# Optimization experiments

Hardware: AMD Instinct MI355X
Metric: run time of the kernel (lower is better)

## Reference

```python
import jax, jax.numpy as jnp
import numpy as np

B, T, I, F, M, O = 256, 512, 128, 512, 512, 128


def setup_inputs() -> dict:
    key = jax.random.key(0)
    ks = jax.random.split(key, 12)
    def lin(k, out_d, in_d):
        std = 1.0 / np.sqrt(in_d)
        kw, kb = jax.random.split(k)
        W = jax.random.uniform(kw, (out_d, in_d), jnp.float32, -std, std)
        b = jax.random.uniform(kb, (out_d,), jnp.float32, -std, std)
        return W, b
    Wi2f, bi2f = lin(ks[0], F, I)
    Wm2f, bm2f = lin(ks[1], F, M)
    Wf2m, bf2m = lin(ks[2], M, F)
    Wm2m, bm2m = lin(ks[3], M, M)
    Wout, bout = lin(ks[4], O, M)
    x = jax.random.normal(ks[5], (B, T, I), jnp.float32)
    m0 = jnp.zeros((B, M), jnp.float32)
    return {"x": x, "m0": m0,
            "Wi2f": Wi2f, "bi2f": bi2f, "Wm2f": Wm2f, "bm2f": bm2f,
            "Wf2m": Wf2m, "bf2m": bf2m, "Wm2m": Wm2m, "bm2m": bm2m,
            "Wout": Wout, "bout": bout}


def reference(x, m0, Wi2f, bi2f, Wm2f, bm2f, Wf2m, bf2m, Wm2m, bm2m, Wout, bout):
    # Precompute input->functional projection for all timesteps (batched GEMM).
    xp = jnp.einsum('bti,fi->btf', x, Wi2f) + bi2f  # (B, T, F)

    def step(m, xp_t):
        f = jnp.tanh(xp_t + m @ Wm2f.T + bm2f)           # (B, F)
        m_new = (f @ Wf2m.T + bf2m) + (m @ Wm2m.T + bm2m)  # (B, M)
        return m_new, m_new

    m_last, _ms = jax.lax.scan(step, m0, jnp.swapaxes(xp, 0, 1))  # ms: (T, B, M)
    # OUTPUT_TYPE.LAST_OUT: output layer applied to final memory state.
    return m_last @ Wout.T + bout  # (B, O)
```

## Files before the change

kernel.cpp:

```cpp
#include <hip/hip_runtime.h>
#include <hip/hip_bf16.h>

typedef __bf16 bf16x8 __attribute__((ext_vector_type(8)));
typedef __bf16 bf16x4 __attribute__((ext_vector_type(4)));
typedef float  f32x4  __attribute__((ext_vector_type(4)));
typedef unsigned int u32;
typedef unsigned long long u64;

static __device__ __forceinline__ void mfma_z(f32x4& d, bf16x8 a, const f32x4& b) {
    asm("v_mfma_f32_16x16x32_bf16 %0, %1, %2, 0"
        : "=&v"(d) : "v"(a), "a"(b));
}
static __device__ __forceinline__ void mfma_a(f32x4& d, bf16x8 a, const f32x4& b) {
    asm("v_mfma_f32_16x16x32_bf16 %0, %1, %2, %0"
        : "+v"(d) : "v"(a), "a"(b));
}
#define ACC_GUARD(e, o) asm volatile("s_nop 7\n\ts_nop 7" : "+v"(e), "+v"(o))

static __device__ __forceinline__ f32x4 mfma16(bf16x8 a, bf16x8 b, f32x4 c) {
    return __builtin_amdgcn_mfma_f32_16x16x32_bf16(a, b, c, 0, 0, 0);
}

static __device__ __forceinline__ void poll_flags(const u32* flags, u32 tgt,
                                                  int lane, u32& alive) {
    if (!alive) return;
    for (u32 it = 0; it < (1u << 22); ++it) {
        u32 v = __hip_atomic_load(&flags[lane & 7], __ATOMIC_RELAXED, __HIP_MEMORY_SCOPE_AGENT);
        if (__all((int)(v >= tgt))) return;
    }
    alive = 0;
}

#define TLEN 512
#define IDIM 128
#define FDIM 512
#define MDIM 512
#define ODIM 128
#define BC   16
#define NGRP 16
#define NCU  8
#define PSTR 520
#define XSTR 136
#define SSTR 20

#define WS_WI   0
#define WS_W2F  (WS_WI  + FDIM*IDIM*2)
#define WS_W2M  (WS_W2F + FDIM*MDIM*2)
#define WS_WF2  (WS_W2M + MDIM*MDIM*2)
#define WS_WO   (WS_WF2 + MDIM*FDIM*2)
#define WS_C    (WS_WO  + ODIM*MDIM*2)
#define WS_D    (WS_C   + FDIM*FDIM*2)
#define WS_B1   (WS_D   + MDIM*FDIM*2)
#define WS_B23  (WS_B1  + FDIM*4)
#define WS_CB   (WS_B23 + MDIM*4)
#define WS_CU   (WS_CB  + FDIM*4)
#define WS_FLG  (WS_CU  + MDIM*4)
#define WS_BUF  (WS_FLG + NGRP*64*4)

#define N_WI  (FDIM*IDIM)
#define N_W2F (FDIM*MDIM)
#define N_W2M (MDIM*MDIM)
#define N_WF2 (MDIM*FDIM)
#define N_WO  (ODIM*MDIM)

__global__ __launch_bounds__(256) void lmn_prep1(
    const float* __restrict__ Wi2f, const float* __restrict__ Wm2f,
    const float* __restrict__ Wm2m, const float* __restrict__ Wf2m,
    const float* __restrict__ Wout,
    const float* __restrict__ bi2f, const float* __restrict__ bm2f,
    const float* __restrict__ bf2m, const float* __restrict__ bm2m,
    __bf16* __restrict__ WI, __bf16* __restrict__ W2F, __bf16* __restrict__ W2M,
    __bf16* __restrict__ WF2, __bf16* __restrict__ WO,
    float* __restrict__ b1, float* __restrict__ b23, u32* __restrict__ flags)
{
    int i = blockIdx.x * 256 + threadIdx.x;
    if (i < N_WI)  { WI[i]  = (__bf16)Wi2f[i]; return; }  i -= N_WI;
    if (i < N_W2F) { W2F[i] = (__bf16)Wm2f[i]; return; }  i -= N_W2F;
    if (i < N_W2M) { W2M[i] = (__bf16)Wm2m[i]; return; }  i -= N_W2M;
    if (i < N_WF2) { WF2[i] = (__bf16)Wf2m[i]; return; }  i -= N_WF2;
    if (i < N_WO)  { WO[i]  = (__bf16)Wout[i]; return; }  i -= N_WO;
    if (i < FDIM)  { b1[i]  = bi2f[i] + bm2f[i]; return; } i -= FDIM;
    if (i < MDIM)  { b23[i] = bf2m[i] + bm2m[i]; return; } i -= MDIM;
    if (i < NGRP * 64) { flags[i] = 0u; return; }
}

__global__ __launch_bounds__(256) void lmn_prep2(
    const float* __restrict__ Wm2f, const float* __restrict__ Wm2m,
    const float* __restrict__ Wf2m,
    const float* __restrict__ b1, const float* __restrict__ b23,
    __bf16* __restrict__ C, __bf16* __restrict__ D,
    float* __restrict__ cb, float* __restrict__ cu)
{
    int bb = blockIdx.x;
    if (bb < 2048) {
        int row = bb >> 1;
        int k   = (bb & 1) * 256 + threadIdx.x;
        const float* A = (row < 512) ? Wm2f : Wm2m;
        int r = row & 511;
        float acc = 0.f;
        for (int j = 0; j < 512; ++j)
            acc += A[(size_t)r * 512 + j] * Wf2m[(size_t)j * 512 + k];
        if (row < 512) C[(size_t)r * 512 + k] = (__bf16)acc;
        else           D[(size_t)r * 512 + k] = (__bf16)acc;
        return;
    }
    int idx = (bb - 2048) * 256 + threadIdx.x;
    if (idx < 512) {
        float acc = b1[idx];
        for (int j = 0; j < 512; ++j) acc += Wm2f[(size_t)idx * 512 + j] * b23[j];
        cb[idx] = acc;
    } else {
        int r = idx - 512;
        float acc = 0.f;
        for (int j = 0; j < 512; ++j) acc += Wm2m[(size_t)r * 512 + j] * b23[j];
        cu[r] = acc;
    }
}

__global__ __launch_bounds__(512, 2) void lmn_scan(
    const float* __restrict__ x, const float* __restrict__ m0,
    const __bf16* __restrict__ WI, const __bf16* __restrict__ W2F,
    const __bf16* __restrict__ W2M, const __bf16* __restrict__ Cm,
    const __bf16* __restrict__ Dm, const __bf16* __restrict__ WF2,
    const __bf16* __restrict__ WO,
    const float* __restrict__ b1, const float* __restrict__ cb,
    const float* __restrict__ cu, const float* __restrict__ b23,
    const float* __restrict__ bout,
    u32* __restrict__ flags_all, __bf16* __restrict__ buf,
    float* __restrict__ out)
{
    __shared__ __bf16 ulds[BC][PSTR];
    __shared__ __bf16 flds[BC][PSTR];
    __shared__ __bf16 xlds[BC][XSTR];
    __shared__ __bf16 sstg[8][BC][SSTR];

    const int tid  = threadIdx.x;
    const int lane = tid & 63;
    const int w    = tid >> 6;
    const int wq   = w & 3;
    const int l15  = lane & 15;
    const int l4   = lane >> 4;
    const int koff = 8 * l4;
    const bool sRole = (w < 4);

    const int b = blockIdx.x;
    const int g = b & 15;
    const int p = b >> 4;
    const int row0 = g * BC;

    u32* flags = flags_all + g * 64;
    u32  alive = 1;

    const int c0 = 64 * p + 16 * wq + l15;

    f32x4 wgt[36];
    {
        const __bf16* rA = (sRole ? W2F : W2M) + (size_t)c0 * MDIM;
        const __bf16* rC = (sRole ? Cm  : Dm ) + (size_t)c0 * FDIM;
        #pragma unroll
        for (int j = 0; j < 16; ++j) {
            wgt[j]      = *(const f32x4*)&rA[j * 32 + koff];
            wgt[16 + j] = *(const f32x4*)&rC[j * 32 + koff];
        }
        if (sRole) {
            const __bf16* rX = WI + (size_t)c0 * IDIM;
            #pragma unroll
            for (int j = 0; j < 4; ++j) wgt[32 + j] = *(const f32x4*)&rX[j * 32 + koff];
        } else {
            #pragma unroll
            for (int j = 32; j < 36; ++j) wgt[j] = f32x4{0, 0, 0, 0};
        }
        #pragma unroll
        for (int j = 0; j < 36; ++j) asm volatile("" : "+a"(wgt[j]));
    }
    const float b1r = sRole ? b1[c0] : 0.f;
    const float cbr = sRole ? cb[c0] : 0.f;
    const float cur = sRole ? 0.f    : cu[c0];

    #pragma unroll
    for (int i = 0; i < 2; ++i) {
        int c = tid + 512 * i;
        int row = c >> 6, col8 = (c & 63) << 3;
        const float* ms = &m0[(size_t)(row0 + row) * MDIM + col8];
        float4 v0 = ((const float4*)ms)[0], v1 = ((const float4*)ms)[1];
        *(bf16x8*)&ulds[row][col8] =
            bf16x8{(__bf16)v0.x, (__bf16)v0.y, (__bf16)v0.z, (__bf16)v0.w,
                   (__bf16)v1.x, (__bf16)v1.y, (__bf16)v1.z, (__bf16)v1.w};
    }
    if (tid < 256) {
        int rr = tid >> 4, c8 = (tid & 15) << 3;
        const float* xs = &x[(size_t)(row0 + rr) * TLEN * IDIM + c8];
        float4 v0 = ((const float4*)xs)[0], v1 = ((const float4*)xs)[1];
        *(bf16x8*)&xlds[rr][c8] =
            bf16x8{(__bf16)v0.x, (__bf16)v0.y, (__bf16)v0.z, (__bf16)v0.w,
                   (__bf16)v1.x, (__bf16)v1.y, (__bf16)v1.z, (__bf16)v1.w};
    }
    __syncthreads();

    f32x4 accE, accO;
    {
        bf16x8 a0 = *(const bf16x8*)&ulds[l15][0 * 32 + koff];
        bf16x8 a1 = *(const bf16x8*)&ulds[l15][1 * 32 + koff];
        mfma_z(accE, a0, wgt[0]);  mfma_z(accO, a1, wgt[1]);
        #pragma unroll
        for (int j = 2; j < 16; ++j) {
            bf16x8 am = *(const bf16x8*)&ulds[l15][j * 32 + koff];
            if (j & 1) mfma_a(accO, am, wgt[j]);
            else       mfma_a(accE, am, wgt[j]);
        }
        if (sRole) {
            #pragma unroll
            for (int j = 0; j < 4; ++j) {
                bf16x8 ax = *(const bf16x8*)&xlds[l15][j * 32 + koff];
                if (j & 1) mfma_a(accO, ax, wgt[32 + j]);
                else       mfma_a(accE, ax, wgt[32 + j]);
            }
        }
    }

    const int erow = lane & 15;
    const int eq4  = lane >> 4;

    for (int t = 0; t < TLEN; ++t) {
        ACC_GUARD(accE, accO);
        f32x4 va = accE + accO;
        if (sRole) {
            const float addc = (t == 0) ? b1r : cbr;
            #pragma unroll
            for (int r = 0; r < 4; ++r)
                sstg[w][4 * l4 + r][l15] = (__bf16)tanhf(va[r] + addc);
        } else {
            const float addu = (t == 0) ? 0.f : cur;
            #pragma unroll
            for (int r = 0; r < 4; ++r)
                sstg[w][4 * l4 + r][l15] = (__bf16)(va[r] + addu);
        }
        asm volatile("s_waitcnt lgkmcnt(0)" ::: "memory");

        const size_t bufbase = (size_t)((t & 1) * NGRP + g) * (2 * BC * MDIM);
        {
            const int mat = sRole ? 1 : 0;
            u64 v = *(const u64*)&sstg[w][erow][4 * eq4];
            __bf16* dst = buf + bufbase + (size_t)mat * (BC * MDIM)
                        + erow * MDIM + 64 * p + 16 * wq + 4 * eq4;
            __hip_atomic_store((u64*)dst, v, __ATOMIC_RELAXED, __HIP_MEMORY_SCOPE_AGENT);
        }
        asm volatile("s_waitcnt vmcnt(0)" ::: "memory");
        __syncthreads();
        if (tid == 0)
            __hip_atomic_store(&flags[p], (u32)t + 1u,
                               __ATOMIC_RELAXED, __HIP_MEMORY_SCOPE_AGENT);

        if (tid < 256 && t + 1 < TLEN) {
            int rr = tid >> 4, c8 = (tid & 15) << 3;
            const float* xs = &x[((size_t)(row0 + rr) * TLEN + (t + 1)) * IDIM + c8];
            float4 v0 = ((const float4*)xs)[0], v1 = ((const float4*)xs)[1];
            *(bf16x8*)&xlds[rr][c8] =
                bf16x8{(__bf16)v0.x, (__bf16)v0.y, (__bf16)v0.z, (__bf16)v0.w,
                       (__bf16)v1.x, (__bf16)v1.y, (__bf16)v1.z, (__bf16)v1.w};
        }
        poll_flags(flags, (u32)t + 1u, lane, alive);

        #pragma unroll
        for (int i = 0; i < 4; ++i) {
            int c = tid + 512 * i;
            int mat = c >> 10, rem = c & 1023;
            int row = rem >> 6, col8 = (rem & 63) << 3;
            const __bf16* src = buf + bufbase + (size_t)mat * (BC * MDIM)
                              + row * MDIM + col8;
            u64 lo = __hip_atomic_load((const u64*)src,     __ATOMIC_RELAXED, __HIP_MEMORY_SCOPE_AGENT);
            u64 hi = __hip_atomic_load((const u64*)src + 1, __ATOMIC_RELAXED, __HIP_MEMORY_SCOPE_AGENT);
            union { u64 q[2]; bf16x8 v; } uu; uu.q[0] = lo; uu.q[1] = hi;
            if (mat) *(bf16x8*)&flds[row][col8] = uu.v;
            else     *(bf16x8*)&ulds[row][col8] = uu.v;
        }
        __syncthreads();

        if (t == TLEN - 1) break;

        {
            bf16x8 a0 = *(const bf16x8*)&ulds[l15][0 * 32 + koff];
            bf16x8 a1 = *(const bf16x8*)&ulds[l15][1 * 32 + koff];
            mfma_z(accE, a0, wgt[0]);  mfma_z(accO, a1, wgt[1]);
            #pragma unroll
            for (int j = 2; j < 16; ++j) {
                bf16x8 am = *(const bf16x8*)&ulds[l15][j * 32 + koff];
                if (j & 1) mfma_a(accO, am, wgt[j]);
                else       mfma_a(accE, am, wgt[j]);
            }
            #pragma unroll
            for (int j = 0; j < 16; ++j) {
                bf16x8 af = *(const bf16x8*)&flds[l15][j * 32 + koff];
                if (j & 1) mfma_a(accO, af, wgt[16 + j]);
                else       mfma_a(accE, af, wgt[16 + j]);
            }
            if (sRole) {
                #pragma unroll
                for (int j = 0; j < 4; ++j) {
                    bf16x8 ax = *(const bf16x8*)&xlds[l15][j * 32 + koff];
                    if (j & 1) mfma_a(accO, ax, wgt[32 + j]);
                    else       mfma_a(accE, ax, wgt[32 + j]);
                }
            }
        }
    }

    if (p == 0) {
        f32x4 ma[4];
        #pragma unroll
        for (int nt = 0; nt < 4; ++nt) {
            int ct = 64 * w + 16 * nt + l15;
            f32x4 acc = {0, 0, 0, 0};
            #pragma unroll
            for (int j = 0; j < 16; ++j) {
                bf16x8 af = *(const bf16x8*)&flds[l15][j * 32 + koff];
                bf16x8 bw = *(const bf16x8*)&WF2[(size_t)ct * FDIM + j * 32 + koff];
                acc = mfma16(af, bw, acc);
            }
            ma[nt] = acc;
        }
        #pragma unroll
        for (int nt = 0; nt < 4; ++nt) {
            int ct = 64 * w + 16 * nt + l15;
            #pragma unroll
            for (int r = 0; r < 4; ++r) {
                float mv = ma[nt][r] + (float)ulds[4 * l4 + r][ct] + b23[ct];
                ulds[4 * l4 + r][ct] = (__bf16)mv;
            }
        }
        __syncthreads();
        const int oc = 16 * w + l15;
        const __bf16* ro = WO + (size_t)oc * MDIM;
        f32x4 oe = {0, 0, 0, 0}, oo = {0, 0, 0, 0};
        #pragma unroll
        for (int j = 0; j < 16; ++j) {
            bf16x8 am = *(const bf16x8*)&ulds[l15][j * 32 + koff];
            bf16x8 bw = *(const bf16x8*)&ro[j * 32 + koff];
            if (j & 1) oo = mfma16(am, bw, oo); else oe = mfma16(am, bw, oe);
        }
        f32x4 oa = oe + oo;
        const float bo = bout[oc];
        #pragma unroll
        for (int r = 0; r < 4; ++r)
            out[(size_t)(row0 + 4 * l4 + r) * ODIM + oc] = oa[r] + bo;
    }
}

extern "C" void kernel_launch(void* const* d_in, const int* in_sizes, int n_in,
                              void* d_out, int out_size, void* d_ws, size_t ws_size,
                              hipStream_t stream)
{
    const float* x    = (const float*)d_in[0];
    const float* m0   = (const float*)d_in[1];
    const float* Wi2f = (const float*)d_in[2];
    const float* bi2f = (const float*)d_in[3];
    const float* Wm2f = (const float*)d_in[4];
    const float* bm2f = (const float*)d_in[5];
    const float* Wf2m = (const float*)d_in[6];
    const float* bf2m = (const float*)d_in[7];
    const float* Wm2m = (const float*)d_in[8];
    const float* bm2m = (const float*)d_in[9];
    const float* Wout = (const float*)d_in[10];
    const float* bout = (const float*)d_in[11];

    char* ws = (char*)d_ws;
    __bf16* WI  = (__bf16*)(ws + WS_WI);
    __bf16* W2F = (__bf16*)(ws + WS_W2F);
    __bf16* W2M = (__bf16*)(ws + WS_W2M);
    __bf16* WF2 = (__bf16*)(ws + WS_WF2);
    __bf16* WO  = (__bf16*)(ws + WS_WO);
    __bf16* Cm  = (__bf16*)(ws + WS_C);
    __bf16* Dm  = (__bf16*)(ws + WS_D);
    float*  b1  = (float*)(ws + WS_B1);
    float*  b23 = (float*)(ws + WS_B23);
    float*  cb  = (float*)(ws + WS_CB);
    float*  cu  = (float*)(ws + WS_CU);
    u32*    flg = (u32*)(ws + WS_FLG);
    __bf16* buf = (__bf16*)(ws + WS_BUF);

    const int prep1_total = N_WI + N_W2F + N_W2M + N_WF2 + N_WO
                          + FDIM + MDIM + NGRP * 64;
    lmn_prep1<<<(prep1_total + 255) / 256, 256, 0, stream>>>(
        Wi2f, Wm2f, Wm2m, Wf2m, Wout, bi2f, bm2f, bf2m, bm2m,
        WI, W2F, W2M, WF2, WO, b1, b23, flg);

    lmn_prep2<<<2052, 256, 0, stream>>>(Wm2f, Wm2m, Wf2m, b1, b23, Cm, Dm, cb, cu);

    lmn_scan<<<NGRP * NCU, 512, 0, stream>>>(
        x, m0, WI, W2F, W2M, Cm, Dm, WF2, WO,
        b1, cb, cu, b23, bout, flg, buf, (float*)d_out);
}
```

Measured before the change: 1.853 ms.

## Halve batch rows per group to 8 and consume own-slice state early from LDS

Batch rows per group drop from 16 to 8, doubling the number of groups to 32 and so the blocks running the recurrence in parallel. MFMA A-operands duplicate the 8 rows across the 16-row tile. The K-loop is rotated per block so each block's own 64-column slice of the new state comes first and is multiplied straight from the staging LDS before the cross-block flag wait. This hides part of the sync latency, at the cost of wasting half of each MFMA on duplicated rows.

```diff
diff --git a/kernel.cpp b/kernel.cpp
--- a/kernel.cpp
+++ b/kernel.cpp
@@ -36,12 +36,12 @@
 #define FDIM 512
 #define MDIM 512
 #define ODIM 128
-#define BC   16
-#define NGRP 16
+#define BC   8
+#define NGRP 32
 #define NCU  8
 #define PSTR 520
 #define XSTR 136
-#define SSTR 20
+#define SSTR 24
 
 #define WS_WI   0
 #define WS_W2F  (WS_WI  + FDIM*IDIM*2)
@@ -141,11 +141,12 @@
     const int l15  = lane & 15;
     const int l4   = lane >> 4;
     const int koff = 8 * l4;
+    const int ar   = l15 & 7;
     const bool sRole = (w < 4);
 
     const int b = blockIdx.x;
-    const int g = b & 15;
-    const int p = b >> 4;
+    const int g = b & 31;
+    const int p = b >> 5;
     const int row0 = g * BC;
 
     u32* flags = flags_all + g * 64;
@@ -159,8 +160,9 @@
         const __bf16* rC = (sRole ? Cm  : Dm ) + (size_t)c0 * FDIM;
         #pragma unroll
         for (int j = 0; j < 16; ++j) {
-            wgt[j]      = *(const f32x4*)&rA[j * 32 + koff];
-            wgt[16 + j] = *(const f32x4*)&rC[j * 32 + koff];
+            int kk = (2 * p + j) & 15;
+            wgt[j]      = *(const f32x4*)&rA[kk * 32 + koff];
+            wgt[16 + j] = *(const f32x4*)&rC[kk * 32 + koff];
         }
         if (sRole) {
             const __bf16* rX = WI + (size_t)c0 * IDIM;
@@ -177,17 +179,15 @@
     const float cbr = sRole ? cb[c0] : 0.f;
     const float cur = sRole ? 0.f    : cu[c0];
 
-    #pragma unroll
-    for (int i = 0; i < 2; ++i) {
-        int c = tid + 512 * i;
-        int row = c >> 6, col8 = (c & 63) << 3;
+    {
+        int row = tid >> 6, col8 = (tid & 63) << 3;
         const float* ms = &m0[(size_t)(row0 + row) * MDIM + col8];
         float4 v0 = ((const float4*)ms)[0], v1 = ((const float4*)ms)[1];
         *(bf16x8*)&ulds[row][col8] =
             bf16x8{(__bf16)v0.x, (__bf16)v0.y, (__bf16)v0.z, (__bf16)v0.w,
                    (__bf16)v1.x, (__bf16)v1.y, (__bf16)v1.z, (__bf16)v1.w};
     }
-    if (tid < 256) {
+    if (tid < 128) {
         int rr = tid >> 4, c8 = (tid & 15) << 3;
         const float* xs = &x[(size_t)(row0 + rr) * TLEN * IDIM + c8];
         float4 v0 = ((const float4*)xs)[0], v1 = ((const float4*)xs)[1];
@@ -199,50 +199,50 @@
 
     f32x4 accE, accO;
     {
-        bf16x8 a0 = *(const bf16x8*)&ulds[l15][0 * 32 + koff];
-        bf16x8 a1 = *(const bf16x8*)&ulds[l15][1 * 32 + koff];
+        bf16x8 a0 = *(const bf16x8*)&ulds[ar][((2 * p + 0) & 15) * 32 + koff];
+        bf16x8 a1 = *(const bf16x8*)&ulds[ar][((2 * p + 1) & 15) * 32 + koff];
         mfma_z(accE, a0, wgt[0]);  mfma_z(accO, a1, wgt[1]);
         #pragma unroll
         for (int j = 2; j < 16; ++j) {
-            bf16x8 am = *(const bf16x8*)&ulds[l15][j * 32 + koff];
+            bf16x8 am = *(const bf16x8*)&ulds[ar][((2 * p + j) & 15) * 32 + koff];
             if (j & 1) mfma_a(accO, am, wgt[j]);
             else       mfma_a(accE, am, wgt[j]);
         }
         if (sRole) {
             #pragma unroll
             for (int j = 0; j < 4; ++j) {
-                bf16x8 ax = *(const bf16x8*)&xlds[l15][j * 32 + koff];
+                bf16x8 ax = *(const bf16x8*)&xlds[ar][j * 32 + koff];
                 if (j & 1) mfma_a(accO, ax, wgt[32 + j]);
                 else       mfma_a(accE, ax, wgt[32 + j]);
             }
         }
     }
-
-    const int erow = lane & 15;
-    const int eq4  = lane >> 4;
 
     for (int t = 0; t < TLEN; ++t) {
         ACC_GUARD(accE, accO);
         f32x4 va = accE + accO;
-        if (sRole) {
-            const float addc = (t == 0) ? b1r : cbr;
-            #pragma unroll
-            for (int r = 0; r < 4; ++r)
-                sstg[w][4 * l4 + r][l15] = (__bf16)tanhf(va[r] + addc);
-        } else {
-            const float addu = (t == 0) ? 0.f : cur;
-            #pragma unroll
-            for (int r = 0; r < 4; ++r)
-                sstg[w][4 * l4 + r][l15] = (__bf16)(va[r] + addu);
+        if (l4 < 2) {
+            if (sRole) {
+                const float addc = (t == 0) ? b1r : cbr;
+                #pragma unroll
+                for (int r = 0; r < 4; ++r)
+                    sstg[w][4 * l4 + r][l15] = (__bf16)tanhf(va[r] + addc);
+            } else {
+                const float addu = (t == 0) ? 0.f : cur;
+                #pragma unroll
+                for (int r = 0; r < 4; ++r)
+                    sstg[w][4 * l4 + r][l15] = (__bf16)(va[r] + addu);
+            }
         }
         asm volatile("s_waitcnt lgkmcnt(0)" ::: "memory");
 
         const size_t bufbase = (size_t)((t & 1) * NGRP + g) * (2 * BC * MDIM);
-        {
-            const int mat = sRole ? 1 : 0;
-            u64 v = *(const u64*)&sstg[w][erow][4 * eq4];
+        if (lane < 32) {
+            const int mat  = sRole ? 1 : 0;
+            const int erow = lane & 7, eq = lane >> 3;
+            u64 v = *(const u64*)&sstg[w][erow][4 * eq];
             __bf16* dst = buf + bufbase + (size_t)mat * (BC * MDIM)
-                        + erow * MDIM + 64 * p + 16 * wq + 4 * eq4;
+                        + erow * MDIM + 64 * p + 16 * wq + 4 * eq;
             __hip_atomic_store((u64*)dst, v, __ATOMIC_RELAXED, __HIP_MEMORY_SCOPE_AGENT);
         }
         asm volatile("s_waitcnt vmcnt(0)" ::: "memory");
@@ -251,7 +251,17 @@
             __hip_atomic_store(&flags[p], (u32)t + 1u,
                                __ATOMIC_RELAXED, __HIP_MEMORY_SCOPE_AGENT);
 
-        if (tid < 256 && t + 1 < TLEN) {
+        if (t + 1 < TLEN) {
+            const int cc = 8 * (l4 & 1);
+            bf16x8 au0 = *(const bf16x8*)&sstg[4 + (l4 >> 1)][ar][cc];
+            bf16x8 au1 = *(const bf16x8*)&sstg[6 + (l4 >> 1)][ar][cc];
+            bf16x8 af0 = *(const bf16x8*)&sstg[0 + (l4 >> 1)][ar][cc];
+            bf16x8 af1 = *(const bf16x8*)&sstg[2 + (l4 >> 1)][ar][cc];
+            mfma_z(accE, au0, wgt[0]);   mfma_z(accO, au1, wgt[1]);
+            mfma_a(accE, af0, wgt[16]);  mfma_a(accO, af1, wgt[17]);
+        }
+
+        if (tid < 128 && t + 1 < TLEN) {
             int rr = tid >> 4, c8 = (tid & 15) << 3;
             const float* xs = &x[((size_t)(row0 + rr) * TLEN + (t + 1)) * IDIM + c8];
             float4 v0 = ((const float4*)xs)[0], v1 = ((const float4*)xs)[1];
@@ -261,43 +271,40 @@
         }
         poll_flags(flags, (u32)t + 1u, lane, alive);
 
-        #pragma unroll
-        for (int i = 0; i < 4; ++i) {
-            int c = tid + 512 * i;
-            int mat = c >> 10, rem = c & 1023;
-            int row = rem >> 6, col8 = (rem & 63) << 3;
+        {
+            int mat = tid >> 8, rem = tid & 255;
+            int row = rem >> 5, col16 = (rem & 31) << 4;
             const __bf16* src = buf + bufbase + (size_t)mat * (BC * MDIM)
-                              + row * MDIM + col8;
-            u64 lo = __hip_atomic_load((const u64*)src,     __ATOMIC_RELAXED, __HIP_MEMORY_SCOPE_AGENT);
-            u64 hi = __hip_atomic_load((const u64*)src + 1, __ATOMIC_RELAXED, __HIP_MEMORY_SCOPE_AGENT);
-            union { u64 q[2]; bf16x8 v; } uu; uu.q[0] = lo; uu.q[1] = hi;
-            if (mat) *(bf16x8*)&flds[row][col8] = uu.v;
-            else     *(bf16x8*)&ulds[row][col8] = uu.v;
+                              + row * MDIM + col16;
+            u64 q0 = __hip_atomic_load((const u64*)src,     __ATOMIC_RELAXED, __HIP_MEMORY_SCOPE_AGENT);
+            u64 q1 = __hip_atomic_load((const u64*)src + 1, __ATOMIC_RELAXED, __HIP_MEMORY_SCOPE_AGENT);
+            u64 q2 = __hip_atomic_load((const u64*)src + 2, __ATOMIC_RELAXED, __HIP_MEMORY_SCOPE_AGENT);
+            u64 q3 = __hip_atomic_load((const u64*)src + 3, __ATOMIC_RELAXED, __HIP_MEMORY_SCOPE_AGENT);
+            __bf16* dl = mat ? &flds[row][col16] : &ulds[row][col16];
+            ((u64*)dl)[0] = q0; ((u64*)dl)[1] = q1;
+            ((u64*)dl)[2] = q2; ((u64*)dl)[3] = q3;
         }
         __syncthreads();
 
         if (t == TLEN - 1) break;
 
         {
-            bf16x8 a0 = *(const bf16x8*)&ulds[l15][0 * 32 + koff];
-            bf16x8 a1 = *(const bf16x8*)&ulds[l15][1 * 32 + koff];
-            mfma_z(accE, a0, wgt[0]);  mfma_z(accO, a1, wgt[1]);
             #pragma unroll
             for (int j = 2; j < 16; ++j) {
-                bf16x8 am = *(const bf16x8*)&ulds[l15][j * 32 + koff];
+                bf16x8 am = *(const bf16x8*)&ulds[ar][((2 * p + j) & 15) * 32 + koff];
                 if (j & 1) mfma_a(accO, am, wgt[j]);
                 else       mfma_a(accE, am, wgt[j]);
             }
             #pragma unroll
-            for (int j = 0; j < 16; ++j) {
-                bf16x8 af = *(const bf16x8*)&flds[l15][j * 32 + koff];
+            for (int j = 2; j < 16; ++j) {
+                bf16x8 af = *(const bf16x8*)&flds[ar][((2 * p + j) & 15) * 32 + koff];
                 if (j & 1) mfma_a(accO, af, wgt[16 + j]);
                 else       mfma_a(accE, af, wgt[16 + j]);
             }
             if (sRole) {
                 #pragma unroll
                 for (int j = 0; j < 4; ++j) {
-                    bf16x8 ax = *(const bf16x8*)&xlds[l15][j * 32 + koff];
+                    bf16x8 ax = *(const bf16x8*)&xlds[ar][j * 32 + koff];
                     if (j & 1) mfma_a(accO, ax, wgt[32 + j]);
                     else       mfma_a(accE, ax, wgt[32 + j]);
                 }
@@ -313,7 +320,7 @@
             f32x4 acc = {0, 0, 0, 0};
             #pragma unroll
             for (int j = 0; j < 16; ++j) {
-                bf16x8 af = *(const bf16x8*)&flds[l15][j * 32 + koff];
+                bf16x8 af = *(const bf16x8*)&flds[ar][j * 32 + koff];
                 bf16x8 bw = *(const bf16x8*)&WF2[(size_t)ct * FDIM + j * 32 + koff];
                 acc = mfma16(af, bw, acc);
             }
@@ -322,10 +329,13 @@
         #pragma unroll
         for (int nt = 0; nt < 4; ++nt) {
             int ct = 64 * w + 16 * nt + l15;
-            #pragma unroll
-            for (int r = 0; r < 4; ++r) {
-                float mv = ma[nt][r] + (float)ulds[4 * l4 + r][ct] + b23[ct];
-                ulds[4 * l4 + r][ct] = (__bf16)mv;
+            if (l4 < 2) {
+                #pragma unroll
+                for (int r = 0; r < 4; ++r) {
+                    int rr = 4 * l4 + r;
+                    float mv = ma[nt][r] + (float)ulds[rr][ct] + b23[ct];
+                    ulds[rr][ct] = (__bf16)mv;
+                }
             }
         }
         __syncthreads();
@@ -334,15 +344,19 @@
         f32x4 oe = {0, 0, 0, 0}, oo = {0, 0, 0, 0};
         #pragma unroll
         for (int j = 0; j < 16; ++j) {
-            bf16x8 am = *(const bf16x8*)&ulds[l15][j * 32 + koff];
+            bf16x8 am = *(const bf16x8*)&ulds[ar][j * 32 + koff];
             bf16x8 bw = *(const bf16x8*)&ro[j * 32 + koff];
             if (j & 1) oo = mfma16(am, bw, oo); else oe = mfma16(am, bw, oe);
         }
         f32x4 oa = oe + oo;
         const float bo = bout[oc];
-        #pragma unroll
-        for (int r = 0; r < 4; ++r)
-            out[(size_t)(row0 + 4 * l4 + r) * ODIM + oc] = oa[r] + bo;
+        if (l4 < 2) {
+            #pragma unroll
+            for (int r = 0; r < 4; ++r) {
+                int rr = 4 * l4 + r;
+                out[(size_t)(row0 + rr) * ODIM + oc] = oa[r] + bo;
+            }
+        }
     }
 }
 
```

After: 1.537 ms. -17.1%, faster.
